# Kernel tuning notes

Hardware: AMD Instinct MI355X
Metric: run time of the kernel (lower is better)

The kernel has to match this reference:

```python
import jax, jax.numpy as jnp
import numpy as np

B, S, D, H, DFF = 4, 2048, 512, 8, 2048
HD = D // H  # head dim = 64
LN_EPS = 1e-5


def setup_inputs() -> dict:
    key = jax.random.key(0)
    ks = jax.random.split(key, 12)
    sc = 0.02
    return {
        "x": jax.random.normal(ks[0], (B, S, D), jnp.float32),
        "Wq": jax.random.normal(ks[1], (D, D), jnp.float32) * sc,
        "bq": jnp.zeros((D,), jnp.float32),
        "Wk": jax.random.normal(ks[2], (D, D), jnp.float32) * sc,
        "bk": jnp.zeros((D,), jnp.float32),
        "Wv": jax.random.normal(ks[3], (D, D), jnp.float32) * sc,
        "bv": jnp.zeros((D,), jnp.float32),
        "W1": jax.random.normal(ks[4], (D, DFF), jnp.float32) * sc,
        "b1": jnp.zeros((DFF,), jnp.float32),
        "W2": jax.random.normal(ks[5], (DFF, D), jnp.float32) * sc,
        "b2": jnp.zeros((D,), jnp.float32),
        "gamma": jnp.ones((D,), jnp.float32),
        "beta": jnp.zeros((D,), jnp.float32),
    }


def reference(x, Wq, bq, Wk, bk, Wv, bv, W1, b1, W2, b2, gamma, beta):
    # Multi-head self-attention (explicit bmm -> softmax -> bmm chain)
    q = (x @ Wq + bq).reshape(B, S, H, HD)
    k = (x @ Wk + bk).reshape(B, S, H, HD)
    v = (x @ Wv + bv).reshape(B, S, H, HD)
    scores = jnp.einsum("bqhd,bkhd->bhqk", q, k) / jnp.sqrt(jnp.float32(HD))
    atn = jax.nn.softmax(scores, axis=-1)          # [B,H,S,S]
    attn_out = jnp.einsum("bhqk,bkhd->bqhd", atn, v).reshape(B, S, D)
    # FFN with residual + LayerNorm (residual around FFN only, as in source)
    h = jax.nn.relu(attn_out @ W1 + b1)
    y = h @ W2 + b2 + attn_out
    mu = jnp.mean(y, axis=-1, keepdims=True)
    var = jnp.var(y, axis=-1, keepdims=True)
    out = (y - mu) * jax.lax.rsqrt(var + LN_EPS) * gamma + beta
    return (out, atn)
```

## Files before the change

kernel.cpp:

```cpp
#include <hip/hip_runtime.h>
#include <hip/hip_bf16.h>

#define TPB 256
typedef long long ll;


using short8  = __attribute__((ext_vector_type(8))) short;
using short4v = __attribute__((ext_vector_type(4))) short;
using floatx4 = __attribute__((ext_vector_type(4))) float;

__device__ __forceinline__ unsigned short f2bu(float f) {
    union { float f; unsigned int u; } v; v.f = f;
    unsigned int u = v.u;
    return (unsigned short)((u + 0x7fffu + ((u >> 16) & 1u)) >> 16);
}

__device__ __forceinline__ float bu2f(unsigned short us) {
    union { unsigned int u; float f; } v; v.u = ((unsigned int)us) << 16;
    return v.f;
}

__device__ __forceinline__ unsigned int cvtpk(float lo, float hi) {
    unsigned int r;
    asm volatile("v_cvt_pk_bf16_f32 %0, %1, %2" : "=v"(r) : "v"(lo), "v"(hi));
    return r;
}

__device__ __forceinline__ float fexp2(float x) {
#if __has_builtin(__builtin_amdgcn_exp2f)
    return __builtin_amdgcn_exp2f(x);
#else
    float r;
    asm("v_exp_f32 %0, %1" : "=v"(r) : "v"(x));
    return r;
#endif
}

__device__ __forceinline__ floatx4 mfma16(short4v a, short4v b, floatx4 c) {
#if __has_builtin(__builtin_amdgcn_mfma_f32_16x16x16bf16_1k)
    return __builtin_amdgcn_mfma_f32_16x16x16bf16_1k(a, b, c, 0, 0, 0);
#else
    floatx4 d;
    asm volatile("v_mfma_f32_16x16x16_bf16 %0, %1, %2, %3"
                 : "=v"(d) : "v"(a), "v"(b), "v"(c));
    return d;
#endif
}

__device__ __forceinline__ void gload16(const unsigned short* g, unsigned short* l) {
    __builtin_amdgcn_global_load_lds(
        (const __attribute__((address_space(1))) void*)g,
        (__attribute__((address_space(3))) void*)l, 16, 0, 0);
}

#define QSCALE 0.18033688f

template<int BM, int BN, int EPI>
__device__ __forceinline__ void gemm_body(
    const unsigned short* __restrict__ Ap, const unsigned short* __restrict__ BTp,
    const float* __restrict__ bias, void* __restrict__ Cp,
    const unsigned short* __restrict__ Rb,
    int K, ll lda, ll ldb, ll ldc, int bx, int by,
    unsigned short* Asm, unsigned short* Bsm)
{
    constexpr int BK = 64;
    const int tid  = threadIdx.x;
    const int lane = tid & 63;
    const int wave = tid >> 6;
    const int wm = wave >> 1, wn = wave & 1;
    constexpr int WM = BM / 2, WN = BN / 2, FM = WM / 16, FN = WN / 16;

    const ll brow = (ll)bx * BM;
    const ll bcol = (ll)by * BN;
    const int srow = lane >> 3;
    const int ssw  = (((lane & 7) ^ srow)) << 3;
    const int kswz = (lane & 7) << 3;

    floatx4 acc[FM][FN] = {};

    for (int k0 = 0; k0 < K; k0 += BK) {
        #pragma unroll
        for (int ii = 0; ii < BM / 32; ++ii) {
            int i = wave + ii * 4;
            gload16(Ap + (brow + i * 8 + srow) * lda + k0 + ssw, Asm + i * 512);
        }
        #pragma unroll
        for (int ii = 0; ii < BN / 32; ++ii) {
            int i = wave + ii * 4;
            gload16(BTp + (bcol + i * 8 + srow) * ldb + k0 + ssw, Bsm + i * 512);
        }
        __syncthreads();

        #pragma unroll
        for (int kk = 0; kk < BK; kk += 32) {
            short8 af[FM], bfr[FN];
            const int kidx = (kk + ((lane >> 4) << 3)) ^ kswz;
            const int ar = wm * WM + (lane & 15);
            const int bc = wn * WN + (lane & 15);
            #pragma unroll
            for (int m = 0; m < FM; m++)
                af[m] = *(const short8*)&Asm[(ar + m * 16) * BK + kidx];
            #pragma unroll
            for (int n = 0; n < FN; n++)
                bfr[n] = *(const short8*)&Bsm[(bc + n * 16) * BK + kidx];
            #pragma unroll
            for (int m = 0; m < FM; m++)
                #pragma unroll
                for (int n = 0; n < FN; n++)
                    acc[m][n] = __builtin_amdgcn_mfma_f32_16x16x32_bf16(af[m], bfr[n], acc[m][n], 0, 0, 0);
        }
        __syncthreads();
    }

    const ll crow0 = brow + wm * WM + ((lane >> 4) << 2);
    const ll ccol0 = bcol + wn * WN + (lane & 15);
    #pragma unroll
    for (int m = 0; m < FM; m++) {
        #pragma unroll
        for (int j = 0; j < 4; j++) {
            ll row = crow0 + m * 16 + j;
            #pragma unroll
            for (int np = 0; np < FN; np += 2) {
                ll col0 = ccol0 + np * 16;
                ll col1 = col0 + 16;
                float v0 = acc[m][np][j]     + bias[col0];
                float v1 = acc[m][np + 1][j] + bias[col1];
                if constexpr (EPI == 3) {
                    v0 = v0 > 0.f ? v0 : 0.f;
                    v1 = v1 > 0.f ? v1 : 0.f;
                } else if constexpr (EPI == 6) {
                    v0 += bu2f(Rb[row * ldc + col0]);
                    v1 += bu2f(Rb[row * ldc + col1]);
                } else if constexpr (EPI == 7) {
                    if (col0 < 512) v0 *= QSCALE;
                    if (col1 < 512) v1 *= QSCALE;
                }
                unsigned int r = cvtpk(v0, v1);
                ((unsigned short*)Cp)[row * ldc + col0] = (unsigned short)r;
                ((unsigned short*)Cp)[row * ldc + col1] = (unsigned short)(r >> 16);
            }
        }
    }
}

template<int BM, int BN, int EPI>
__global__ __launch_bounds__(TPB) void gemm_k(
    const unsigned short* __restrict__ Ap, const unsigned short* __restrict__ BTp,
    const float* __restrict__ bias, void* __restrict__ Cp,
    const unsigned short* __restrict__ Rb,
    int K, ll lda, ll ldb, ll ldc)
{
    __shared__ unsigned short sh[BM * 64 + BN * 64];
    int nwg = gridDim.x * gridDim.y;
    int sid = blockIdx.y * gridDim.x + blockIdx.x;
    int cpx = nwg >> 3;
    int w = (sid & 7) * cpx + (sid >> 3);
    int bx = w % gridDim.x, by = w / gridDim.x;
    gemm_body<BM, BN, EPI>(Ap, BTp, bias, Cp, Rb, K, lda, ldb, ldc, bx, by,
                           sh, sh + BM * 64);
}

__device__ __forceinline__ void atnwrite_body(
    const unsigned short* __restrict__ qkv, const float* __restrict__ ilbuf,
    float* __restrict__ atn, int bh, int qt, unsigned short* sh)
{
    unsigned short* Qsm = sh;
    unsigned short* Ksm = sh + 8192;
    float* Pst = (float*)sh;

    const int tid = threadIdx.x, lane = tid & 63, wave = tid >> 6;
    const int c0 = lane & 15, g = lane >> 4;
    const int b = bh >> 3, h = bh & 7;

    const ll qbase  = ((ll)(b * 2048 + qt * 128)) * 1536 + h * 64;
    const ll kbase0 = ((ll)(b * 2048)) * 1536 + 512 + h * 64;
    const int srow = lane >> 3;
    const int ssw  = (((lane & 7) ^ srow)) << 3;
    const int kswz = (lane & 7) << 3;

    #pragma unroll
    for (int ii = 0; ii < 4; ++ii) {
        int i = wave + ii * 4;
        gload16(qkv + qbase + (ll)(i * 8 + srow) * 1536 + ssw, Qsm + i * 512);
    }
    __syncthreads();
    short8 qf[2][2];
    #pragma unroll
    for (int nq = 0; nq < 2; nq++)
        #pragma unroll
        for (int kk = 0; kk < 2; kk++)
            qf[nq][kk] = *(const short8*)&Qsm[(wave * 32 + nq * 16 + c0) * 64 + ((kk * 32 + g * 8) ^ kswz)];

    float il2[2];
    #pragma unroll
    for (int nq = 0; nq < 2; nq++)
        il2[nq] = ilbuf[(ll)bh * 2048 + qt * 128 + wave * 32 + nq * 16 + c0];

    float* myP = Pst + wave * 1024;

    for (int kb = 0; kb < 16; ++kb) {
        const ll koff = kbase0 + (ll)kb * 128 * 1536;
        #pragma unroll
        for (int ii = 0; ii < 4; ++ii) {
            int i = wave + ii * 4;
            gload16(qkv + koff + (ll)(i * 8 + srow) * 1536 + ssw, Ksm + i * 512);
        }
        __syncthreads();

        floatx4 sacc[8][2] = {};
        #pragma unroll
        for (int kk = 0; kk < 2; kk++)
            #pragma unroll
            for (int mk = 0; mk < 8; mk++) {
                short8 kf = *(const short8*)&Ksm[(mk * 16 + c0) * 64 + ((kk * 32 + g * 8) ^ kswz)];
                #pragma unroll
                for (int nq = 0; nq < 2; nq++)
                    sacc[mk][nq] = __builtin_amdgcn_mfma_f32_16x16x32_bf16(kf, qf[nq][kk], sacc[mk][nq], 0, 0, 0);
            }

        #pragma unroll
        for (int mk = 0; mk < 8; mk++)
            #pragma unroll
            for (int nq = 0; nq < 2; nq++)
                #pragma unroll
                for (int r = 0; r < 4; r++)
                    sacc[mk][nq][r] = fexp2(sacc[mk][nq][r]) * il2[nq];

        #pragma unroll
        for (int nq = 0; nq < 2; nq++) {
            #pragma unroll
            for (int hf = 0; hf < 2; hf++) {
                if ((c0 >> 3) == hf) {
                    int rho = c0 & 7;
                    #pragma unroll
                    for (int mk = 0; mk < 8; mk++) {
                        int k4 = mk * 4 + g;
                        ((floatx4*)myP)[rho * 32 + (k4 ^ rho)] = sacc[mk][nq];
                    }
                }
                const ll grow = (ll)bh * 2048 + qt * 128 + wave * 32 + nq * 16 + hf * 8;
                #pragma unroll
                for (int t = 0; t < 4; t++) {
                    int rr = t * 2 + (lane >> 5);
                    int k4r = lane & 31;
                    floatx4 v = ((const floatx4*)myP)[rr * 32 + (k4r ^ rr)];
                    __builtin_nontemporal_store(
                        v, (floatx4*)(atn + (grow + rr) * 2048 + kb * 128 + k4r * 4));
                }
            }
        }
        __syncthreads();
    }
}

__device__ __forceinline__ void attn1_body(
    const unsigned short* __restrict__ qkv, const unsigned short* __restrict__ vt,
    unsigned short* __restrict__ attnb, float* __restrict__ ilbuf,
    int bh, int qt, unsigned short* sh)
{
    const int tid = threadIdx.x, lane = tid & 63, wave = tid >> 6;
    const int c0 = lane & 15, g = lane >> 4;
    const int srow = lane >> 3;
    const int ssw  = (((lane & 7) ^ srow)) << 3;
    const int kswz = (lane & 7) << 3;
    const int b = bh >> 3, h = bh & 7;

    const ll qbase  = ((ll)(b * 2048 + qt * 128)) * 1536 + h * 64;
    const ll kbase0 = ((ll)(b * 2048)) * 1536 + 512 + h * 64;
    const unsigned short* vbase = vt + (ll)bh * 64 * 2048;

    #pragma unroll
    for (int ii = 0; ii < 4; ++ii) {
        int i = wave + ii * 4;
        gload16(qkv + qbase + (ll)(i * 8 + srow) * 1536 + ssw, sh + i * 512);
    }
    __syncthreads();
    short8 qf[2][2];
    #pragma unroll
    for (int nq = 0; nq < 2; nq++)
        #pragma unroll
        for (int kk = 0; kk < 2; kk++)
            qf[nq][kk] = *(const short8*)&sh[(wave * 32 + nq * 16 + c0) * 64 + ((kk * 32 + g * 8) ^ kswz)];
    __syncthreads();

    floatx4 oaccT[4][2] = {};
    float l_run[2] = {0.f, 0.f};

#define STAGE_KV(kbx, bb) do {                                                   \
    const ll koff_ = kbase0 + (ll)(kbx) * 128 * 1536;                            \
    unsigned short* Kd_ = sh + ((bb) << 13);                                     \
    unsigned short* Vd_ = sh + 16384 + ((bb) << 13);                             \
    _Pragma("unroll")                                                            \
    for (int ii = 0; ii < 4; ++ii) { int i = wave + ii * 4;                      \
        gload16(qkv + koff_ + (ll)(i * 8 + srow) * 1536 + ssw, Kd_ + i * 512); } \
    _Pragma("unroll")                                                            \
    for (int ii = 0; ii < 4; ++ii) { int i = wave + ii * 4; int s = i * 8 + srow;\
        int vrow = s >> 1; int vslot = ((s & 1) << 3) | (lane & 7);              \
        gload16(vbase + (ll)vrow * 2048 + (kbx) * 128 + ((vslot ^ (vrow & 7)) << 3), \
                Vd_ + i * 512); }                                                \
} while (0)

    STAGE_KV(0, 0);
    for (int kb = 0; kb < 16; ++kb) {
        const int cur = kb & 1;
        if (kb < 15) {
            STAGE_KV(kb + 1, cur ^ 1);
            asm volatile("s_waitcnt vmcnt(8)" ::: "memory");
        } else {
            asm volatile("s_waitcnt vmcnt(0)" ::: "memory");
        }
        __builtin_amdgcn_sched_barrier(0);
        __builtin_amdgcn_s_barrier();
        __builtin_amdgcn_sched_barrier(0);

        unsigned short* Kc = sh + (cur << 13);
        unsigned short* Vc = sh + 16384 + (cur << 13);

        floatx4 sacc[8][2] = {};
        #pragma unroll
        for (int kk = 0; kk < 2; kk++)
            #pragma unroll
            for (int mk = 0; mk < 8; mk++) {
                short8 kf = *(const short8*)&Kc[(mk * 16 + c0) * 64 + ((kk * 32 + g * 8) ^ kswz)];
                #pragma unroll
                for (int nq = 0; nq < 2; nq++)
                    sacc[mk][nq] = __builtin_amdgcn_mfma_f32_16x16x32_bf16(kf, qf[nq][kk], sacc[mk][nq], 0, 0, 0);
            }

        #pragma unroll
        for (int nq = 0; nq < 2; nq++) {
            float rs = 0.f;
            #pragma unroll
            for (int mk = 0; mk < 8; mk++)
                #pragma unroll
                for (int r = 0; r < 4; r++) {
                    float p = fexp2(sacc[mk][nq][r]);
                    sacc[mk][nq][r] = p;
                    rs += p;
                }
            rs += __shfl_xor(rs, 16);
            rs += __shfl_xor(rs, 32);
            l_run[nq] += rs;
        }

        #pragma unroll
        for (int mk = 0; mk < 8; mk++) {
            short4v pb[2];
            #pragma unroll
            for (int nq = 0; nq < 2; nq++) {
                union { unsigned int u[2]; short4v s; } pu;
                pu.u[0] = cvtpk(sacc[mk][nq][0], sacc[mk][nq][1]);
                pu.u[1] = cvtpk(sacc[mk][nq][2], sacc[mk][nq][3]);
                pb[nq] = pu.s;
            }
            #pragma unroll
            for (int mk2 = 0; mk2 < 4; mk2++) {
                short4v vf = *(const short4v*)&Vc[(mk2 * 16 + c0) * 128 + ((mk * 16 + g * 4) ^ kswz)];
                #pragma unroll
                for (int nq = 0; nq < 2; nq++)
                    oaccT[mk2][nq] = mfma16(vf, pb[nq], oaccT[mk2][nq]);
            }
        }
        __builtin_amdgcn_sched_barrier(0);
        __builtin_amdgcn_s_barrier();
        __builtin_amdgcn_sched_barrier(0);
    }
#undef STAGE_KV

    const float il[2] = { 1.0f / l_run[0], 1.0f / l_run[1] };

    #pragma unroll
    for (int nq = 0; nq < 2; nq++) {
        int qrow = qt * 128 + wave * 32 + nq * 16 + c0;
        ll row = (ll)b * 2048 + qrow;
        #pragma unroll
        for (int mk2 = 0; mk2 < 4; mk2++) {
            int col = h * 64 + mk2 * 16 + g * 4;
            unsigned int r0 = cvtpk(oaccT[mk2][nq][0] * il[nq], oaccT[mk2][nq][1] * il[nq]);
            unsigned int r1 = cvtpk(oaccT[mk2][nq][2] * il[nq], oaccT[mk2][nq][3] * il[nq]);
            int2 tb = { (int)r0, (int)r1 };
            *(int2*)&attnb[row * 512 + col] = tb;
        }
        if (g == 0) ilbuf[(ll)bh * 2048 + qrow] = il[nq];
    }
}

__global__ __launch_bounds__(TPB) void attn1a_k(
    const unsigned short* __restrict__ qkv, const unsigned short* __restrict__ vt,
    unsigned short* __restrict__ attnb, float* __restrict__ ilbuf)
{
    __shared__ unsigned short sh[32768];
    const int n = blockIdx.x;
    const int bh = (n & 7) * 2 + ((n >> 3) & 1);
    const int qt = n >> 4;
    attn1_body(qkv, vt, attnb, ilbuf, bh, qt, sh);
}

__global__ __launch_bounds__(TPB) void fused1_k(
    const unsigned short* __restrict__ qkv, const unsigned short* __restrict__ vt,
    unsigned short* __restrict__ attnb, float* __restrict__ ilbuf,
    float* __restrict__ atn)
{
    __shared__ unsigned short sh[32768];
    const int bid = blockIdx.x;
    if (bid < 128) {
        atnwrite_body(qkv, ilbuf, atn, bid & 7, bid >> 3, sh);
    } else {
        const int m = bid - 128;
        const int bh = 16 + (m & 7) * 2 + ((m >> 3) & 1);
        const int qt = m >> 4;
        attn1_body(qkv, vt, attnb, ilbuf, bh, qt, sh);
    }
}

template<int WRBH0, int WRCNT, int GX, int GY, int BM, int BN, int EPI>
__global__ __launch_bounds__(TPB) void fusedg_k(
    const unsigned short* __restrict__ qkv, const float* __restrict__ ilbuf,
    float* __restrict__ atn,
    const unsigned short* __restrict__ Ap, const unsigned short* __restrict__ BTp,
    const float* __restrict__ bias, void* __restrict__ Cp,
    const unsigned short* __restrict__ Rb,
    int K, ll lda, ll ldb, ll ldc)
{
    __shared__ unsigned short sh[16384];
    const int bid = blockIdx.x;
    constexpr int WRN = WRCNT * 16;
    if (bid < WRN) {
        atnwrite_body(qkv, ilbuf, atn, WRBH0 + bid % WRCNT, bid / WRCNT, sh);
    } else {
        int sid = bid - WRN;
        constexpr int NWG = GX * GY;
        int w = (sid & 7) * (NWG >> 3) + (sid >> 3);
        int bx = w % GX, by = w / GX;
        gemm_body<BM, BN, EPI>(Ap, BTp, bias, Cp, Rb, K, lda, ldb, ldc, bx, by,
                               sh, sh + BM * 64);
    }
}

__global__ __launch_bounds__(TPB) void ln_k(const unsigned short* __restrict__ y,
                                            const float* __restrict__ gamma,
                                            const float* __restrict__ beta,
                                            float* __restrict__ out)
{
    const int lane = threadIdx.x & 63;
    const ll row = (ll)blockIdx.x * 4 + (threadIdx.x >> 6);
    short8 v = *(const short8*)(y + row * 512 + lane * 8);
    float f[8];
    float s = 0.f, q = 0.f;
    #pragma unroll
    for (int j = 0; j < 8; j++) {
        f[j] = bu2f((unsigned short)v[j]);
        s += f[j]; q += f[j] * f[j];
    }
    #pragma unroll
    for (int off = 32; off; off >>= 1) { s += __shfl_xor(s, off); q += __shfl_xor(q, off); }
    const float mu  = s * (1.0f / 512.0f);
    const float var = q * (1.0f / 512.0f) - mu * mu;
    const float rs  = rsqrtf(var + 1e-5f);

    float4 g0 = *(const float4*)(gamma + lane * 8);
    float4 g1 = *(const float4*)(gamma + lane * 8 + 4);
    float4 e0 = *(const float4*)(beta  + lane * 8);
    float4 e1 = *(const float4*)(beta  + lane * 8 + 4);
    floatx4 o0, o1;
    o0[0] = (f[0] - mu) * rs * g0.x + e0.x;  o0[1] = (f[1] - mu) * rs * g0.y + e0.y;
    o0[2] = (f[2] - mu) * rs * g0.z + e0.z;  o0[3] = (f[3] - mu) * rs * g0.w + e0.w;
    o1[0] = (f[4] - mu) * rs * g1.x + e1.x;  o1[1] = (f[5] - mu) * rs * g1.y + e1.y;
    o1[2] = (f[6] - mu) * rs * g1.z + e1.z;  o1[3] = (f[7] - mu) * rs * g1.w + e1.w;
    __builtin_nontemporal_store(o0, (floatx4*)(out + row * 512 + lane * 8));
    __builtin_nontemporal_store(o1, (floatx4*)(out + row * 512 + lane * 8 + 4));
}

__global__ __launch_bounds__(TPB) void prep_k(
    const float* __restrict__ Wq, const float* __restrict__ Wk,
    const float* __restrict__ Wv, const float* __restrict__ W1,
    const float* __restrict__ W2,
    const float* __restrict__ bq, const float* __restrict__ bk,
    const float* __restrict__ bv, const float* __restrict__ x,
    unsigned short* __restrict__ wtqkv, unsigned short* __restrict__ wt1,
    unsigned short* __restrict__ wt2, float* __restrict__ bqkv,
    unsigned short* __restrict__ xb)
{
    __shared__ float t[32 * 33];
    const int bid = blockIdx.x;
    const float* W; unsigned short* WT; int K, N, tile;
    if (bid < 256)       { W = Wq; WT = wtqkv;             K = 512;  N = 512;  tile = bid; }
    else if (bid < 512)  { W = Wk; WT = wtqkv + 512 * 512; K = 512;  N = 512;  tile = bid - 256; }
    else if (bid < 768)  { W = Wv; WT = wtqkv + 1024 * 512;K = 512;  N = 512;  tile = bid - 512; }
    else if (bid < 1792) { W = W1; WT = wt1;               K = 512;  N = 2048; tile = bid - 768; }
    else if (bid < 2816) { W = W2; WT = wt2;               K = 2048; N = 512;  tile = bid - 1792; }
    else if (bid < 2822) {
        int i = (bid - 2816) * TPB + threadIdx.x;
        if (i < 512)       bqkv[i] = bq[i];
        else if (i < 1024) bqkv[i] = bk[i - 512];
        else if (i < 1536) bqkv[i] = bv[i - 1024];
        return;
    } else {
        ll i = ((ll)(bid - 2822) * TPB + threadIdx.x) * 4;
        float4 v = *(const float4*)(x + i);
        unsigned int r0 = cvtpk(v.x, v.y), r1 = cvtpk(v.z, v.w);
        int2 tt = { (int)r0, (int)r1 };
        *(int2*)(xb + i) = tt;
        return;
    }
    const int nx = N >> 5;
    const int n0 = (tile % nx) * 32, k0 = (tile / nx) * 32;
    const int tx = threadIdx.x & 31, ty = threadIdx.x >> 5;
    #pragma unroll
    for (int i = ty; i < 32; i += 8) t[i * 33 + tx] = W[(ll)(k0 + i) * N + n0 + tx];
    __syncthreads();
    #pragma unroll
    for (int i = ty; i < 32; i += 8) WT[(ll)(n0 + i) * K + k0 + tx] = f2bu(t[tx * 33 + i]);
}

__global__ __launch_bounds__(TPB) void transv_k(const unsigned short* __restrict__ qkv,
                                                unsigned short* __restrict__ vt)
{
    const int z = blockIdx.y;  const int b = z >> 3, h = z & 7;
    const int s0 = blockIdx.x * 64;
    __shared__ unsigned short t[64][72];
    const unsigned short* src = qkv + ((ll)(b * 2048 + s0)) * 1536 + 1024 + h * 64;
    for (int c = threadIdx.x; c < 512; c += TPB) {
        int r = c >> 3, c8 = (c & 7) << 3;
        *(int4*)&t[r][c8] = *(const int4*)(src + (ll)r * 1536 + c8);
    }
    __syncthreads();
    unsigned short* dst = vt + (ll)z * 64 * 2048 + s0;
    for (int c = threadIdx.x; c < 512; c += TPB) {
        int hd = c >> 3, s8 = (c & 7) << 3;
        unsigned short tmp[8];
        #pragma unroll
        for (int j = 0; j < 8; j++) tmp[j] = t[s8 + j][hd];
        *(int4*)(dst + (ll)hd * 2048 + s8) = *(const int4*)tmp;
    }
}

extern "C" void kernel_launch(void* const* d_in, const int* in_sizes, int n_in,
                              void* d_out, int out_size, void* d_ws, size_t ws_size,
                              hipStream_t stream)
{
    (void)in_sizes; (void)n_in; (void)out_size; (void)ws_size;
    const float* x     = (const float*)d_in[0];
    const float* Wq    = (const float*)d_in[1];
    const float* bq    = (const float*)d_in[2];
    const float* Wk    = (const float*)d_in[3];
    const float* bk    = (const float*)d_in[4];
    const float* Wv    = (const float*)d_in[5];
    const float* bv    = (const float*)d_in[6];
    const float* W1    = (const float*)d_in[7];
    const float* b1    = (const float*)d_in[8];
    const float* W2    = (const float*)d_in[9];
    const float* b2    = (const float*)d_in[10];
    const float* gamma = (const float*)d_in[11];
    const float* beta  = (const float*)d_in[12];

    char* ws = (char*)d_ws;
    size_t off = 0;
    auto alloc = [&](size_t bytes) -> char* {
        char* p = ws + off; off += (bytes + 255) & ~(size_t)255; return p;
    };
    unsigned short* xb    = (unsigned short*)alloc(8192ll * 512 * 2);
    unsigned short* wtqkv = (unsigned short*)alloc(1536ll * 512 * 2);
    unsigned short* wt1   = (unsigned short*)alloc(2048ll * 512 * 2);
    unsigned short* wt2   = (unsigned short*)alloc(512ll * 2048 * 2);
    float*          bqkv  = (float*)alloc(1536 * 4);
    unsigned short* qkv   = (unsigned short*)alloc(8192ll * 1536 * 2);
    unsigned short* vt    = (unsigned short*)alloc(32ll * 64 * 2048 * 2);
    unsigned short* attnb = (unsigned short*)alloc(8192ll * 512 * 2);
    unsigned short* hmid  = (unsigned short*)alloc(8192ll * 2048 * 2);
    unsigned short* ybuf  = (unsigned short*)alloc(8192ll * 512 * 2);
    float*          ilbuf = (float*)alloc(32ll * 2048 * 4);

    float* outp = (float*)d_out;
    float* atn  = outp + 4194304;

    prep_k<<<2822 + 4096, TPB, 0, stream>>>(Wq, Wk, Wv, W1, W2, bq, bk, bv, x,
                                            wtqkv, wt1, wt2, bqkv, xb);

    gemm_k<128, 128, 7><<<dim3(64, 12, 1), TPB, 0, stream>>>(
        xb, wtqkv, bqkv, qkv, nullptr, 512, 512, 512, 1536);

    transv_k<<<dim3(32, 32), TPB, 0, stream>>>(qkv, vt);

    attn1a_k<<<256, TPB, 0, stream>>>(qkv, vt, attnb, ilbuf);

    fused1_k<<<384, TPB, 0, stream>>>(qkv, vt, attnb, ilbuf, atn);

    fusedg_k<8, 12, 64, 16, 128, 128, 3><<<192 + 1024, TPB, 0, stream>>>(
        qkv, ilbuf, atn,
        attnb, wt1, b1, hmid, nullptr, 512, 512, 512, 2048);

    fusedg_k<20, 12, 128, 4, 64, 128, 6><<<192 + 512, TPB, 0, stream>>>(
        qkv, ilbuf, atn,
        hmid, wt2, b2, ybuf, attnb, 2048, 2048, 2048, 512);

    ln_k<<<2048, TPB, 0, stream>>>(ybuf, gamma, beta, outp);
}
```

Measured before the change: 271.6 us.

## Fuse V transpose into QKV GEMM epilogue and merge attention into one 512-thread kernel

The QKV GEMM epilogue now writes the V columns straight into the transposed vt layout, which removes the separate transpose kernel. The two attention launches (attn1a and the attention half of fused1) are replaced by one 512-thread kernel that handles 256 query rows per block across all 32 batch-heads. The atn-write tiles are redistributed across the two fused GEMM kernels (start offsets and counts changed). The cost is that the V writes become 8-byte strided stores and the larger blocks may lower occupancy.

```diff
diff --git a/kernel.cpp b/kernel.cpp
--- a/kernel.cpp
+++ b/kernel.cpp
@@ -59,7 +59,7 @@
 __device__ __forceinline__ void gemm_body(
     const unsigned short* __restrict__ Ap, const unsigned short* __restrict__ BTp,
     const float* __restrict__ bias, void* __restrict__ Cp,
-    const unsigned short* __restrict__ Rb,
+    const unsigned short* __restrict__ Rb, unsigned short* __restrict__ Vtp,
     int K, ll lda, ll ldb, ll ldc, int bx, int by,
     unsigned short* Asm, unsigned short* Bsm)
 {
@@ -114,6 +114,28 @@
 
     const ll crow0 = brow + wm * WM + ((lane >> 4) << 2);
     const ll ccol0 = bcol + wn * WN + (lane & 15);
+
+    if constexpr (EPI == 7) {
+        if (ccol0 >= 1024) {
+            const int bz = (int)(brow >> 11);
+            #pragma unroll
+            for (int m = 0; m < FM; m++) {
+                const int sl = (int)((crow0 + m * 16) & 2047);
+                #pragma unroll
+                for (int n = 0; n < FN; n++) {
+                    const int col = (int)(ccol0 + n * 16);
+                    const float bv = bias[col];
+                    const int hdg = col - 1024;
+                    unsigned int u0 = cvtpk(acc[m][n][0] + bv, acc[m][n][1] + bv);
+                    unsigned int u1 = cvtpk(acc[m][n][2] + bv, acc[m][n][3] + bv);
+                    int2 t = { (int)u0, (int)u1 };
+                    *(int2*)(Vtp + ((ll)((bz * 8 + (hdg >> 6)) * 64 + (hdg & 63))) * 2048 + sl) = t;
+                }
+            }
+            return;
+        }
+    }
+
     #pragma unroll
     for (int m = 0; m < FM; m++) {
         #pragma unroll
@@ -147,7 +169,7 @@
 __global__ __launch_bounds__(TPB) void gemm_k(
     const unsigned short* __restrict__ Ap, const unsigned short* __restrict__ BTp,
     const float* __restrict__ bias, void* __restrict__ Cp,
-    const unsigned short* __restrict__ Rb,
+    const unsigned short* __restrict__ Rb, unsigned short* __restrict__ Vtp,
     int K, ll lda, ll ldb, ll ldc)
 {
     __shared__ unsigned short sh[BM * 64 + BN * 64];
@@ -156,7 +178,7 @@
     int cpx = nwg >> 3;
     int w = (sid & 7) * cpx + (sid >> 3);
     int bx = w % gridDim.x, by = w / gridDim.x;
-    gemm_body<BM, BN, EPI>(Ap, BTp, bias, Cp, Rb, K, lda, ldb, ldc, bx, by,
+    gemm_body<BM, BN, EPI>(Ap, BTp, bias, Cp, Rb, Vtp, K, lda, ldb, ldc, bx, by,
                            sh, sh + BM * 64);
 }
 
@@ -253,25 +275,31 @@
     }
 }
 
-__device__ __forceinline__ void attn1_body(
+__global__ __launch_bounds__(512) void attn8_k(
     const unsigned short* __restrict__ qkv, const unsigned short* __restrict__ vt,
-    unsigned short* __restrict__ attnb, float* __restrict__ ilbuf,
-    int bh, int qt, unsigned short* sh)
-{
-    const int tid = threadIdx.x, lane = tid & 63, wave = tid >> 6;
+    unsigned short* __restrict__ attnb, float* __restrict__ ilbuf)
+{
+    __shared__ unsigned short sh[32768];
+
+    const int tid = threadIdx.x, lane = tid & 63, w = tid >> 6;
     const int c0 = lane & 15, g = lane >> 4;
     const int srow = lane >> 3;
     const int ssw  = (((lane & 7) ^ srow)) << 3;
     const int kswz = (lane & 7) << 3;
+
+    const int n = blockIdx.x;
+    const int j = n >> 3;
+    const int bh = (n & 7) * 4 + (j & 3);
+    const int qp = j >> 2;
     const int b = bh >> 3, h = bh & 7;
 
-    const ll qbase  = ((ll)(b * 2048 + qt * 128)) * 1536 + h * 64;
+    const ll qbase  = ((ll)(b * 2048 + qp * 256)) * 1536 + h * 64;
     const ll kbase0 = ((ll)(b * 2048)) * 1536 + 512 + h * 64;
     const unsigned short* vbase = vt + (ll)bh * 64 * 2048;
 
     #pragma unroll
     for (int ii = 0; ii < 4; ++ii) {
-        int i = wave + ii * 4;
+        int i = w + ii * 8;
         gload16(qkv + qbase + (ll)(i * 8 + srow) * 1536 + ssw, sh + i * 512);
     }
     __syncthreads();
@@ -280,7 +308,7 @@
     for (int nq = 0; nq < 2; nq++)
         #pragma unroll
         for (int kk = 0; kk < 2; kk++)
-            qf[nq][kk] = *(const short8*)&sh[(wave * 32 + nq * 16 + c0) * 64 + ((kk * 32 + g * 8) ^ kswz)];
+            qf[nq][kk] = *(const short8*)&sh[(w * 32 + nq * 16 + c0) * 64 + ((kk * 32 + g * 8) ^ kswz)];
     __syncthreads();
 
     floatx4 oaccT[4][2] = {};
@@ -291,10 +319,10 @@
     unsigned short* Kd_ = sh + ((bb) << 13);                                     \
     unsigned short* Vd_ = sh + 16384 + ((bb) << 13);                             \
     _Pragma("unroll")                                                            \
-    for (int ii = 0; ii < 4; ++ii) { int i = wave + ii * 4;                      \
+    for (int ii = 0; ii < 2; ++ii) { int i = w + ii * 8;                         \
         gload16(qkv + koff_ + (ll)(i * 8 + srow) * 1536 + ssw, Kd_ + i * 512); } \
     _Pragma("unroll")                                                            \
-    for (int ii = 0; ii < 4; ++ii) { int i = wave + ii * 4; int s = i * 8 + srow;\
+    for (int ii = 0; ii < 2; ++ii) { int i = w + ii * 8; int s = i * 8 + srow;   \
         int vrow = s >> 1; int vslot = ((s & 1) << 3) | (lane & 7);              \
         gload16(vbase + (ll)vrow * 2048 + (kbx) * 128 + ((vslot ^ (vrow & 7)) << 3), \
                 Vd_ + i * 512); }                                                \
@@ -305,7 +333,7 @@
         const int cur = kb & 1;
         if (kb < 15) {
             STAGE_KV(kb + 1, cur ^ 1);
-            asm volatile("s_waitcnt vmcnt(8)" ::: "memory");
+            asm volatile("s_waitcnt vmcnt(4)" ::: "memory");
         } else {
             asm volatile("s_waitcnt vmcnt(0)" ::: "memory");
         }
@@ -371,7 +399,7 @@
 
     #pragma unroll
     for (int nq = 0; nq < 2; nq++) {
-        int qrow = qt * 128 + wave * 32 + nq * 16 + c0;
+        int qrow = qp * 256 + w * 32 + nq * 16 + c0;
         ll row = (ll)b * 2048 + qrow;
         #pragma unroll
         for (int mk2 = 0; mk2 < 4; mk2++) {
@@ -382,34 +410,6 @@
             *(int2*)&attnb[row * 512 + col] = tb;
         }
         if (g == 0) ilbuf[(ll)bh * 2048 + qrow] = il[nq];
-    }
-}
-
-__global__ __launch_bounds__(TPB) void attn1a_k(
-    const unsigned short* __restrict__ qkv, const unsigned short* __restrict__ vt,
-    unsigned short* __restrict__ attnb, float* __restrict__ ilbuf)
-{
-    __shared__ unsigned short sh[32768];
-    const int n = blockIdx.x;
-    const int bh = (n & 7) * 2 + ((n >> 3) & 1);
-    const int qt = n >> 4;
-    attn1_body(qkv, vt, attnb, ilbuf, bh, qt, sh);
-}
-
-__global__ __launch_bounds__(TPB) void fused1_k(
-    const unsigned short* __restrict__ qkv, const unsigned short* __restrict__ vt,
-    unsigned short* __restrict__ attnb, float* __restrict__ ilbuf,
-    float* __restrict__ atn)
-{
-    __shared__ unsigned short sh[32768];
-    const int bid = blockIdx.x;
-    if (bid < 128) {
-        atnwrite_body(qkv, ilbuf, atn, bid & 7, bid >> 3, sh);
-    } else {
-        const int m = bid - 128;
-        const int bh = 16 + (m & 7) * 2 + ((m >> 3) & 1);
-        const int qt = m >> 4;
-        attn1_body(qkv, vt, attnb, ilbuf, bh, qt, sh);
     }
 }
 
@@ -432,8 +432,8 @@
         constexpr int NWG = GX * GY;
         int w = (sid & 7) * (NWG >> 3) + (sid >> 3);
         int bx = w % GX, by = w / GX;
-        gemm_body<BM, BN, EPI>(Ap, BTp, bias, Cp, Rb, K, lda, ldb, ldc, bx, by,
-                               sh, sh + BM * 64);
+        gemm_body<BM, BN, EPI>(Ap, BTp, bias, Cp, Rb, nullptr, K, lda, ldb, ldc,
+                               bx, by, sh, sh + BM * 64);
     }
 }
 
@@ -513,28 +513,6 @@
     for (int i = ty; i < 32; i += 8) WT[(ll)(n0 + i) * K + k0 + tx] = f2bu(t[tx * 33 + i]);
 }
 
-__global__ __launch_bounds__(TPB) void transv_k(const unsigned short* __restrict__ qkv,
-                                                unsigned short* __restrict__ vt)
-{
-    const int z = blockIdx.y;  const int b = z >> 3, h = z & 7;
-    const int s0 = blockIdx.x * 64;
-    __shared__ unsigned short t[64][72];
-    const unsigned short* src = qkv + ((ll)(b * 2048 + s0)) * 1536 + 1024 + h * 64;
-    for (int c = threadIdx.x; c < 512; c += TPB) {
-        int r = c >> 3, c8 = (c & 7) << 3;
-        *(int4*)&t[r][c8] = *(const int4*)(src + (ll)r * 1536 + c8);
-    }
-    __syncthreads();
-    unsigned short* dst = vt + (ll)z * 64 * 2048 + s0;
-    for (int c = threadIdx.x; c < 512; c += TPB) {
-        int hd = c >> 3, s8 = (c & 7) << 3;
-        unsigned short tmp[8];
-        #pragma unroll
-        for (int j = 0; j < 8; j++) tmp[j] = t[s8 + j][hd];
-        *(int4*)(dst + (ll)hd * 2048 + s8) = *(const int4*)tmp;
-    }
-}
-
 extern "C" void kernel_launch(void* const* d_in, const int* in_sizes, int n_in,
                               void* d_out, int out_size, void* d_ws, size_t ws_size,
                               hipStream_t stream)
@@ -578,19 +556,15 @@
                                             wtqkv, wt1, wt2, bqkv, xb);
 
     gemm_k<128, 128, 7><<<dim3(64, 12, 1), TPB, 0, stream>>>(
-        xb, wtqkv, bqkv, qkv, nullptr, 512, 512, 512, 1536);
-
-    transv_k<<<dim3(32, 32), TPB, 0, stream>>>(qkv, vt);
-
-    attn1a_k<<<256, TPB, 0, stream>>>(qkv, vt, attnb, ilbuf);
-
-    fused1_k<<<384, TPB, 0, stream>>>(qkv, vt, attnb, ilbuf, atn);
-
-    fusedg_k<8, 12, 64, 16, 128, 128, 3><<<192 + 1024, TPB, 0, stream>>>(
+        xb, wtqkv, bqkv, qkv, nullptr, vt, 512, 512, 512, 1536);
+
+    attn8_k<<<256, 512, 0, stream>>>(qkv, vt, attnb, ilbuf);
+
+    fusedg_k<0, 16, 64, 16, 128, 128, 3><<<256 + 1024, TPB, 0, stream>>>(
         qkv, ilbuf, atn,
         attnb, wt1, b1, hmid, nullptr, 512, 512, 512, 2048);
 
-    fusedg_k<20, 12, 128, 4, 64, 128, 6><<<192 + 512, TPB, 0, stream>>>(
+    fusedg_k<16, 16, 128, 4, 64, 128, 6><<<256 + 512, TPB, 0, stream>>>(
         qkv, ilbuf, atn,
         hmid, wt2, b2, ybuf, attnb, 2048, 2048, 2048, 512);
 
```

After: 260.1 us, median of 3. 4.2% less time.
